# Performance work log

Measured on AMD Instinct MI355X. Metric: run time of the kernel, lower is better.

## Reference

```python
import jax, jax.numpy as jnp
import numpy as np

B, L, D, H = 2, 384, 256, 8
DH = D // H


def setup_inputs() -> dict:
    key = jax.random.key(0)
    ks = jax.random.split(key, 16)
    xav = lambda k, shape: jax.random.normal(k, shape, jnp.float32) * np.sqrt(2.0 / sum(shape[-2:]))
    return {
        "key": jax.random.normal(ks[0], (B, L, D), jnp.float32),
        "query": jax.random.normal(ks[1], (B, L, D), jnp.float32),
        "value": jax.random.normal(ks[2], (B, L, D), jnp.float32),
        "pos": jax.random.normal(ks[3], (B, L, L, D), jnp.float32),
        "key_mask": jnp.ones((B, L), jnp.float32),
        "Wk": xav(ks[4], (D, D)), "bk": jnp.zeros((D,), jnp.float32),
        "Wq": xav(ks[5], (D, D)), "bq": jnp.zeros((D,), jnp.float32),
        "Wv": xav(ks[6], (D, D)), "bv": jnp.zeros((D,), jnp.float32),
        "Wr": xav(ks[7], (D, D)), "br": jnp.zeros((D,), jnp.float32),
        "u": xav(ks[8], (H, DH)),
        "v": xav(ks[9], (H, DH)),
    }


def reference(key, query, value, pos, key_mask, Wk, bk, Wq, bq, Wv, bv, Wr, br, u, v):
    b, l, d = key.shape
    dh = d // H
    # projections (torch Linear: x @ W.T + b)
    k = (key @ Wk.T + bk).reshape(b, l, H, dh).transpose(0, 2, 1, 3)    # [b,h,l,dh]
    q = (query @ Wq.T + bq).reshape(b, l, H, dh).transpose(0, 2, 1, 3)  # [b,h,l,dh]
    val = (value @ Wv.T + bv).reshape(b, l, H, dh).transpose(0, 2, 1, 3)
    r = (pos @ Wr.T + br).reshape(b, l, l, H, dh)                       # [b,q,k,h,dh]
    # content term A+C: (q + u) @ k^T
    A_C = jnp.einsum("bhqd,bhkd->bhqk", q + u[None, :, None, :], k)
    # position term B+D: (q + v) contracted with per-(q,k) relative embedding
    B_D = jnp.einsum("bhqd,bqkhd->bhqk", q + v[None, :, None, :], r)
    score = (A_C + B_D) / np.sqrt(dh).astype(np.float32)
    score = score - (1.0 - key_mask[:, None, None, :]) * 1e15
    attn = jax.nn.softmax(score, axis=-1)  # dropout is identity at eval
    out = jnp.einsum("bhqk,bhkd->bhqd", attn, val)
    return out.transpose(0, 2, 1, 3).reshape(b, l, d)
```

## Files before the change

kernel.cpp:

```cpp
#include <hip/hip_runtime.h>
#include <math.h>

#define BB 2
#define LL 384
#define DD 256
#define HH 8
#define DHH 32

static const size_t OFF_Q   = 0;
static const size_t OFF_KK  = 196608;
static const size_t OFF_VV  = 393216;
static const size_t OFF_W   = 589824;
static const size_t OFF_CBR = 2162688;

__device__ __forceinline__ float dot4(float4 a, float4 b) {
    return a.x * b.x + a.y * b.y + a.z * b.z + a.w * b.w;
}

__global__ __launch_bounds__(256) void k_proj(
    const float* __restrict__ Xq, const float* __restrict__ Xk, const float* __restrict__ Xv,
    const float* __restrict__ Wq, const float* __restrict__ Wk, const float* __restrict__ Wv,
    const float* __restrict__ bq, const float* __restrict__ bk, const float* __restrict__ bv,
    float* __restrict__ oq, float* __restrict__ okk, float* __restrict__ ovv)
{
    int bx = blockIdx.x;
    int mat = bx / 96;
    int rem = bx % 96;
    int b = rem / 48;
    int l0 = (rem % 48) * 8;
    const float* X = (mat == 0) ? Xq : (mat == 1) ? Xk : Xv;
    const float* W = (mat == 0) ? Wq : (mat == 1) ? Wk : Wv;
    const float* bias = (mat == 0) ? bq : (mat == 1) ? bk : bv;

    __shared__ float xs[8 * 256];
    int tid = threadIdx.x;
    {
        const float4* src = (const float4*)(X + (size_t)(b * LL + l0) * DD);
        float4* dst = (float4*)xs;
        dst[tid] = src[tid];
        dst[tid + 256] = src[tid + 256];
    }
    __syncthreads();

    int n = tid;
    float bn = bias[n];
    float acc[8];
#pragma unroll
    for (int l = 0; l < 8; ++l) acc[l] = bn;

    const float4* wrow = (const float4*)(W + (size_t)n * DD);
#pragma unroll 8
    for (int kc = 0; kc < 64; ++kc) {
        float4 wv = wrow[kc];
#pragma unroll
        for (int l = 0; l < 8; ++l) {
            float4 xv = ((const float4*)(xs + l * 256))[kc];
            acc[l] += dot4(wv, xv);
        }
    }

    if (mat == 0) {
#pragma unroll
        for (int l = 0; l < 8; ++l)
            oq[(size_t)(b * LL + l0 + l) * DD + n] = acc[l];
    } else {
        float* o = (mat == 1) ? okk : ovv;
        int h = n >> 5, dh = n & 31;
#pragma unroll
        for (int l = 0; l < 8; ++l)
            o[((size_t)(b * HH + h) * LL + l0 + l) * DHH + dh] = acc[l];
    }
}

__global__ __launch_bounds__(256) void k_wproj(
    const float* __restrict__ q, const float* __restrict__ vpar,
    const float* __restrict__ Wr, const float* __restrict__ br,
    float* __restrict__ w, float* __restrict__ cbr)
{
    int b = blockIdx.x / 96;
    int l0 = (blockIdx.x % 96) * 4;
    int tid = threadIdx.x;
    int gq = tid >> 6;
    int lane = tid & 63;

    __shared__ float qv[4][256];
    {
        const float4* qsrc = (const float4*)(q + (size_t)(b * LL + l0 + gq) * DD);
        const float4* vsrc = (const float4*)vpar;
        float4 t = qsrc[lane];
        float4 vv4 = vsrc[lane];
        t.x += vv4.x; t.y += vv4.y; t.z += vv4.z; t.w += vv4.w;
        ((float4*)qv[gq])[lane] = t;
    }
    __syncthreads();

    int l = l0 + gq;
    int d4 = lane * 4;
    float* wbase = w + ((size_t)(b * LL + l) * HH) * DD + d4;
    for (int h = 0; h < HH; ++h) {
        float4 acc = make_float4(0.f, 0.f, 0.f, 0.f);
#pragma unroll 8
        for (int dh = 0; dh < 32; ++dh) {
            float s = qv[gq][h * 32 + dh];
            float4 wr4 = *(const float4*)(Wr + (size_t)(h * 32 + dh) * DD + d4);
            acc.x += s * wr4.x; acc.y += s * wr4.y; acc.z += s * wr4.z; acc.w += s * wr4.w;
        }
        *(float4*)(wbase + h * DD) = acc;
    }

    if (tid < 32) {
        int g2 = tid >> 3, hh = tid & 7;
        float s = 0.f;
#pragma unroll 8
        for (int dh = 0; dh < 32; ++dh)
            s += qv[g2][hh * 32 + dh] * br[hh * 32 + dh];
        cbr[(size_t)(b * LL + l0 + g2) * HH + hh] = s;
    }
}

__global__ __launch_bounds__(256, 3) void k_fused(
    const float* __restrict__ pos, const float* __restrict__ w,
    const float* __restrict__ q, const float* __restrict__ u,
    const float* __restrict__ kk, const float* __restrict__ vv,
    const float* __restrict__ cbr, const float* __restrict__ mask,
    float* __restrict__ out)
{
    int b = blockIdx.x / LL;
    int qi = blockIdx.x % LL;
    int tid = threadIdx.x;
    int wave = tid >> 6;
    int lane = tid & 63;
    int g = lane & 15;
    int r = lane >> 4;

    __shared__ float sc[HH][LL];
    __shared__ float qu[DD];

    const float inv = 0.17677669529663687f;

    const float* wb = w + ((size_t)(b * LL + qi) * HH) * DD + g * 4;
    float4 wr[8][4];
#pragma unroll
    for (int h = 0; h < 8; ++h) {
#pragma unroll
        for (int j = 0; j < 4; ++j)
            wr[h][j] = *(const float4*)(wb + h * DD + j * 64);
    }

    qu[tid] = q[(size_t)(b * LL + qi) * DD + tid] + u[tid];
    __syncthreads();

    {
        int h = tid >> 5;
        int kb = (tid & 31) * 12;
        float cb = cbr[(size_t)(b * LL + qi) * HH + h];
        const float4* qp = (const float4*)(qu + h * 32);
#pragma unroll 2
        for (int j = 0; j < 12; ++j) {
            int k = kb + j;
            const float4* krow = (const float4*)(kk + ((size_t)(b * HH + h) * LL + k) * DHH);
            float acc = 0.f;
#pragma unroll
            for (int jj = 0; jj < 8; ++jj) acc += dot4(qp[jj], krow[jj]);
            float pen = (1.0f - mask[b * LL + k]) * 1e15f;
            sc[h][k] = (acc + cb) * inv - pen;
        }
    }
    __syncthreads();

    const float* posq = pos + (size_t)(b * LL + qi) * LL * DD + g * 4;
#pragma unroll 1
    for (int k0 = wave * 4; k0 < LL; k0 += 16) {
        int krow = k0 + r;
        const float* pr = posq + (size_t)krow * DD;
        float4 p0 = *(const float4*)(pr);
        float4 p1 = *(const float4*)(pr + 64);
        float4 p2 = *(const float4*)(pr + 128);
        float4 p3 = *(const float4*)(pr + 192);
        float acc[8];
#pragma unroll
        for (int h = 0; h < 8; ++h)
            acc[h] = dot4(p0, wr[h][0]) + dot4(p1, wr[h][1]) +
                     dot4(p2, wr[h][2]) + dot4(p3, wr[h][3]);
#pragma unroll
        for (int m = 1; m <= 8; m <<= 1) {
#pragma unroll
            for (int h = 0; h < 8; ++h)
                acc[h] += __shfl_xor(acc[h], m, 64);
        }
        if (g == 0) {
#pragma unroll
            for (int h = 0; h < 8; ++h)
                sc[h][krow] += acc[h] * inv;
        }
    }
    __syncthreads();

#pragma unroll
    for (int ri = 0; ri < 2; ++ri) {
        int h = wave * 2 + ri;
        float s[6];
#pragma unroll
        for (int j = 0; j < 6; ++j) s[j] = sc[h][lane + 64 * j];
        float m = s[0];
#pragma unroll
        for (int j = 1; j < 6; ++j) m = fmaxf(m, s[j]);
#pragma unroll
        for (int off = 1; off < 64; off <<= 1) m = fmaxf(m, __shfl_xor(m, off, 64));
        float e[6];
        float ls = 0.f;
#pragma unroll
        for (int j = 0; j < 6; ++j) { e[j] = __expf(s[j] - m); ls += e[j]; }
#pragma unroll
        for (int off = 1; off < 64; off <<= 1) ls += __shfl_xor(ls, off, 64);
        float rinv = 1.0f / ls;
#pragma unroll
        for (int j = 0; j < 6; ++j) sc[h][lane + 64 * j] = e[j] * rinv;
    }
    __syncthreads();

    {
        int h = tid >> 5, dh = tid & 31;
        const float* vb = vv + ((size_t)(b * HH + h) * LL) * DHH + dh;
        float acc = 0.f;
#pragma unroll 1
        for (int k = 0; k < LL; k += 4) {
            float v0 = vb[(size_t)(k + 0) * DHH];
            float v1 = vb[(size_t)(k + 1) * DHH];
            float v2 = vb[(size_t)(k + 2) * DHH];
            float v3 = vb[(size_t)(k + 3) * DHH];
            acc += sc[h][k + 0] * v0 + sc[h][k + 1] * v1 +
                   sc[h][k + 2] * v2 + sc[h][k + 3] * v3;
        }
        out[(size_t)(b * LL + qi) * DD + h * 32 + dh] = acc;
    }
}

extern "C" void kernel_launch(void* const* d_in, const int* in_sizes, int n_in,
                              void* d_out, int out_size, void* d_ws, size_t ws_size,
                              hipStream_t stream) {
    const float* key    = (const float*)d_in[0];
    const float* query  = (const float*)d_in[1];
    const float* value  = (const float*)d_in[2];
    const float* pos    = (const float*)d_in[3];
    const float* kmask  = (const float*)d_in[4];
    const float* Wk     = (const float*)d_in[5];
    const float* bk     = (const float*)d_in[6];
    const float* Wq     = (const float*)d_in[7];
    const float* bq     = (const float*)d_in[8];
    const float* Wv     = (const float*)d_in[9];
    const float* bv     = (const float*)d_in[10];
    const float* Wr     = (const float*)d_in[11];
    const float* br     = (const float*)d_in[12];
    const float* u      = (const float*)d_in[13];
    const float* v      = (const float*)d_in[14];
    float* out = (float*)d_out;

    float* ws = (float*)d_ws;
    float* qbuf   = ws + OFF_Q;
    float* kkbuf  = ws + OFF_KK;
    float* vvbuf  = ws + OFF_VV;
    float* wbuf   = ws + OFF_W;
    float* cbrbuf = ws + OFF_CBR;

    k_proj<<<dim3(288), dim3(256), 0, stream>>>(query, key, value, Wq, Wk, Wv,
                                                bq, bk, bv, qbuf, kkbuf, vvbuf);
    k_wproj<<<dim3(192), dim3(256), 0, stream>>>(qbuf, v, Wr, br, wbuf, cbrbuf);
    k_fused<<<dim3(768), dim3(256), 0, stream>>>(pos, wbuf, qbuf, u, kkbuf, vvbuf,
                                                 cbrbuf, kmask, out);
}
```

Measured before the change: 555.9 us.

## Split heads across wave pairs to halve per-thread weight registers in pos stage

In the position-term stage, the heads are now split into two groups of four. Each pair of waves handles one group, so each thread keeps only 4x4 float4 weight registers instead of 8x4. Each wave now processes two key rows per iteration, which keeps more independent pos loads in flight. The trade-off is that every pos row is fetched by two waves, relying on cache hits for the second read. The P·V loop is also unrolled from 4 to 8 loads per iteration to add memory-level parallelism.

```diff
diff --git a/kernel.cpp b/kernel.cpp
--- a/kernel.cpp
+++ b/kernel.cpp
@@ -132,16 +132,18 @@
     int lane = tid & 63;
     int g = lane & 15;
     int r = lane >> 4;
+    int hg = wave >> 1;
+    int kp = wave & 1;
 
     __shared__ float sc[HH][LL];
     __shared__ float qu[DD];
 
     const float inv = 0.17677669529663687f;
 
-    const float* wb = w + ((size_t)(b * LL + qi) * HH) * DD + g * 4;
-    float4 wr[8][4];
-#pragma unroll
-    for (int h = 0; h < 8; ++h) {
+    const float* wb = w + ((size_t)(b * LL + qi) * HH + hg * 4) * DD + g * 4;
+    float4 wr[4][4];
+#pragma unroll
+    for (int h = 0; h < 4; ++h) {
 #pragma unroll
         for (int j = 0; j < 4; ++j)
             wr[h][j] = *(const float4*)(wb + h * DD + j * 64);
@@ -170,28 +172,41 @@
 
     const float* posq = pos + (size_t)(b * LL + qi) * LL * DD + g * 4;
 #pragma unroll 1
-    for (int k0 = wave * 4; k0 < LL; k0 += 16) {
-        int krow = k0 + r;
-        const float* pr = posq + (size_t)krow * DD;
-        float4 p0 = *(const float4*)(pr);
-        float4 p1 = *(const float4*)(pr + 64);
-        float4 p2 = *(const float4*)(pr + 128);
-        float4 p3 = *(const float4*)(pr + 192);
-        float acc[8];
-#pragma unroll
-        for (int h = 0; h < 8; ++h)
-            acc[h] = dot4(p0, wr[h][0]) + dot4(p1, wr[h][1]) +
-                     dot4(p2, wr[h][2]) + dot4(p3, wr[h][3]);
+    for (int k0 = kp * 4; k0 < LL; k0 += 16) {
+        int ka = k0 + r;
+        int kb2 = k0 + 8 + r;
+        const float* pa = posq + (size_t)ka * DD;
+        const float* pb = posq + (size_t)kb2 * DD;
+        float4 a0 = *(const float4*)(pa);
+        float4 a1 = *(const float4*)(pa + 64);
+        float4 a2 = *(const float4*)(pa + 128);
+        float4 a3 = *(const float4*)(pa + 192);
+        float4 b0 = *(const float4*)(pb);
+        float4 b1 = *(const float4*)(pb + 64);
+        float4 b2 = *(const float4*)(pb + 128);
+        float4 b3 = *(const float4*)(pb + 192);
+        float accA[4], accB[4];
+#pragma unroll
+        for (int h = 0; h < 4; ++h) {
+            accA[h] = dot4(a0, wr[h][0]) + dot4(a1, wr[h][1]) +
+                      dot4(a2, wr[h][2]) + dot4(a3, wr[h][3]);
+            accB[h] = dot4(b0, wr[h][0]) + dot4(b1, wr[h][1]) +
+                      dot4(b2, wr[h][2]) + dot4(b3, wr[h][3]);
+        }
 #pragma unroll
         for (int m = 1; m <= 8; m <<= 1) {
 #pragma unroll
-            for (int h = 0; h < 8; ++h)
-                acc[h] += __shfl_xor(acc[h], m, 64);
+            for (int h = 0; h < 4; ++h) {
+                accA[h] += __shfl_xor(accA[h], m, 64);
+                accB[h] += __shfl_xor(accB[h], m, 64);
+            }
         }
         if (g == 0) {
 #pragma unroll
-            for (int h = 0; h < 8; ++h)
-                sc[h][krow] += acc[h] * inv;
+            for (int h = 0; h < 4; ++h) {
+                sc[hg * 4 + h][ka]  += accA[h] * inv;
+                sc[hg * 4 + h][kb2] += accB[h] * inv;
+            }
         }
     }
     __syncthreads();
@@ -224,13 +239,12 @@
         const float* vb = vv + ((size_t)(b * HH + h) * LL) * DHH + dh;
         float acc = 0.f;
 #pragma unroll 1
-        for (int k = 0; k < LL; k += 4) {
-            float v0 = vb[(size_t)(k + 0) * DHH];
-            float v1 = vb[(size_t)(k + 1) * DHH];
-            float v2 = vb[(size_t)(k + 2) * DHH];
-            float v3 = vb[(size_t)(k + 3) * DHH];
-            acc += sc[h][k + 0] * v0 + sc[h][k + 1] * v1 +
-                   sc[h][k + 2] * v2 + sc[h][k + 3] * v3;
+        for (int k = 0; k < LL; k += 8) {
+            float vs[8];
+#pragma unroll
+            for (int j = 0; j < 8; ++j) vs[j] = vb[(size_t)(k + j) * DHH];
+#pragma unroll
+            for (int j = 0; j < 8; ++j) acc += sc[h][k + j] * vs[j];
         }
         out[(size_t)(b * LL + qi) * DD + h * 32 + dh] = acc;
     }
```

After: 537.9 us. 3.2% less time.
